# Optimization experiments

Hardware: AMD Instinct MI355X
Metric: run time of the kernel (lower is better)

Reference implementation:

```python
import jax, jax.numpy as jnp
import numpy as np

I = 8      # input size
H = 128    # hidden size
G = 3 * H  # gate rows (reset, update, new)


def setup_inputs() -> dict:
    key = jax.random.key(0)
    ks = jax.random.split(key, 9)
    s = lambda k, shp: (jax.random.normal(k, shp, jnp.float32) * 0.08)
    return {
        "x": jax.random.normal(ks[0], (1, 32768, I), jnp.float32),
        # layer 0 (input 8 -> hidden 128)
        "w_ih0": s(ks[1], (G, I)),
        "w_hh0": s(ks[2], (G, H)),
        "b_ih0": s(ks[3], (G,)),
        "b_hh0": s(ks[4], (G,)),
        # layer 1 (hidden 128 -> hidden 128)
        "w_ih1": s(ks[5], (G, H)),
        "w_hh1": s(ks[6], (G, H)),
        "b_ih1": s(ks[7], (G,)),
        "b_hh1": s(ks[8], (G,)),
    }


def _gru_cell(h, x, w_ih, w_hh, b_ih, b_hh):
    # PyTorch GRU cell math
    gi = x @ w_ih.T + b_ih          # (G,)
    gh = h @ w_hh.T + b_hh          # (G,)
    i_r, i_z, i_n = jnp.split(gi, 3, axis=-1)
    h_r, h_z, h_n = jnp.split(gh, 3, axis=-1)
    r = jax.nn.sigmoid(i_r + h_r)
    z = jax.nn.sigmoid(i_z + h_z)
    n = jnp.tanh(i_n + r * h_n)
    return (1.0 - z) * n + z * h


def reference(x, w_ih0, w_hh0, b_ih0, b_hh0, w_ih1, w_hh1, b_ih1, b_hh1):
    # Torch loop: for k in range(T): feed x[:, k, :] as a length-L sequence
    # (batch=1), carrying hn across chunks. Equivalent flat step order is
    # (k, l) -> index k*L + l, i.e. swapaxes then flatten.
    L, T, _ = x.shape
    seq = jnp.swapaxes(x, 0, 1).reshape(L * T, I)  # (L*T, 8)

    def step(carry, xt):
        h0, h1 = carry
        h0 = _gru_cell(h0, xt, w_ih0, w_hh0, b_ih0, b_hh0)
        h1 = _gru_cell(h1, h0, w_ih1, w_hh1, b_ih1, b_hh1)
        return (h0, h1), h1

    init = (jnp.zeros((H,), x.dtype), jnp.zeros((H,), x.dtype))
    _, outs = jax.lax.scan(step, init, seq)          # (L*T, H)
    # pred from the final chunk: its L top-layer outputs, shape (L, 1, H)
    return outs[-L:].reshape(L, 1, H)
```

## Files before the change

### kernel.cpp

```cpp
#include <hip/hip_runtime.h>


#define T_STEPS 32768
#define HDIM 128
#define CH 1024
#define NC (T_STEPS / CH)
#define GS 8

typedef __attribute__((ext_vector_type(2))) float f32x2;
typedef __attribute__((ext_vector_type(4))) float f32x4;

__device__ __forceinline__ f32x2 lo2(f32x4 v) { return __builtin_shufflevector(v, v, 0, 1); }
__device__ __forceinline__ f32x2 hi2(f32x4 v) { return __builtin_shufflevector(v, v, 2, 3); }
__device__ __forceinline__ void pkfma(f32x2& acc, f32x2 a, f32x2 b) {
  asm("v_pk_fma_f32 %0, %1, %2, %0" : "+v"(acc) : "v"(a), "v"(b));
}
__device__ __forceinline__ float red8(float v) {
  int t = __builtin_amdgcn_mov_dpp(__builtin_bit_cast(int, v), 0xB1, 0xF, 0xF, true);
  v += __builtin_bit_cast(float, t);
  t = __builtin_amdgcn_mov_dpp(__builtin_bit_cast(int, v), 0x4E, 0xF, 0xF, true);
  v += __builtin_bit_cast(float, t);
  t = __builtin_amdgcn_mov_dpp(__builtin_bit_cast(int, v), 0x141, 0xF, 0xF, true);
  v += __builtin_bit_cast(float, t);
  return v;
}

__global__ __launch_bounds__(256)
void gru_prep(const float* __restrict__ w_ih0, const float* __restrict__ w_hh0,
              const float* __restrict__ b_ih0, const float* __restrict__ b_hh0,
              const float* __restrict__ w_ih1, const float* __restrict__ w_hh1,
              const float* __restrict__ b_ih1, const float* __restrict__ b_hh1,
              float* __restrict__ W0s, float* __restrict__ W1s,
              float* __restrict__ Wi0s, float* __restrict__ Wi1s,
              float* __restrict__ bA0, float* __restrict__ bA1,
              float* __restrict__ bhnS0, float* __restrict__ bhnS1) {
  const float SRZ = -1.4426950408889634f;
  const float SN  =  2.8853900817779268f;
  const int i = blockIdx.x * 256 + threadIdx.x;
  if (i < 49152) {
    const float s = ((i >> 7) < 256) ? SRZ : SN;
    W0s[i]  = w_hh0[i] * s;
    W1s[i]  = w_hh1[i] * s;
    Wi1s[i] = w_ih1[i] * s;
  }
  if (i < 3072) Wi0s[i] = w_ih0[i] * (((i >> 3) < 256) ? SRZ : SN);
  if (i < 384) {
    bA0[i] = (i < 256) ? SRZ * (b_ih0[i] + b_hh0[i]) : SN * b_ih0[i];
    bA1[i] = (i < 256) ? SRZ * (b_ih1[i] + b_hh1[i]) : SN * b_ih1[i];
  }
  if (i < 128) {
    bhnS0[i] = SN * b_hh0[256 + i];
    bhnS1[i] = SN * b_hh1[256 + i];
  }
}

#define PKM(D, A, B) "v_pk_mul_f32 v[" D "], v[" A "], v[" B "]\n\t"
#define PKF(D, A, B) "v_pk_fma_f32 v[" D "], v[" A "], v[" B "], v[" D "]\n\t"

#define DOTROW_A(ACC, W0, W1, W2, W3) \
  PKM(ACC, W0, "60:61") PKF(ACC, W1, "62:63") \
  PKF(ACC, W2, "64:65") PKF(ACC, W3, "66:67")
#define DOTROW_B(ACC, W4, W5, W6, W7) \
  PKF(ACC, W4, "68:69") PKF(ACC, W5, "70:71") \
  PKF(ACC, W6, "72:73") PKF(ACC, W7, "74:75")

#define DOTS6_A \
  DOTROW_A("76:77","100:101","102:103","104:105","106:107") \
  DOTROW_A("78:79","116:117","118:119","120:121","122:123") \
  DOTROW_A("80:81","132:133","134:135","136:137","138:139") \
  DOTROW_A("82:83","148:149","150:151","152:153","154:155") \
  DOTROW_A("84:85","164:165","166:167","168:169","170:171") \
  DOTROW_A("86:87","180:181","182:183","184:185","186:187")
#define DOTS6_B \
  DOTROW_B("76:77","108:109","110:111","112:113","114:115") \
  DOTROW_B("78:79","124:125","126:127","128:129","130:131") \
  DOTROW_B("80:81","140:141","142:143","144:145","146:147") \
  DOTROW_B("82:83","156:157","158:159","160:161","162:163") \
  DOTROW_B("84:85","172:173","174:175","176:177","178:179") \
  DOTROW_B("86:87","188:189","190:191","192:193","194:195")

#define RED6 \
  "v_add_f32 v50, v76, v77\n\t" "v_add_f32 v51, v78, v79\n\t" \
  "v_add_f32 v52, v80, v81\n\t" "v_add_f32 v53, v82, v83\n\t" \
  "v_add_f32 v54, v84, v85\n\t" "v_add_f32 v55, v86, v87\n\t" \
  "v_add_f32 v50, v50, v50 quad_perm:[1,0,3,2]\n\t" \
  "v_add_f32 v51, v51, v51 quad_perm:[1,0,3,2]\n\t" \
  "v_add_f32 v52, v52, v52 quad_perm:[1,0,3,2]\n\t" \
  "v_add_f32 v53, v53, v53 quad_perm:[1,0,3,2]\n\t" \
  "v_add_f32 v54, v54, v54 quad_perm:[1,0,3,2]\n\t" \
  "v_add_f32 v55, v55, v55 quad_perm:[1,0,3,2]\n\t" \
  "v_add_f32 v50, v50, v50 quad_perm:[2,3,0,1]\n\t" \
  "v_add_f32 v51, v51, v51 quad_perm:[2,3,0,1]\n\t" \
  "v_add_f32 v52, v52, v52 quad_perm:[2,3,0,1]\n\t" \
  "v_add_f32 v53, v53, v53 quad_perm:[2,3,0,1]\n\t" \
  "v_add_f32 v54, v54, v54 quad_perm:[2,3,0,1]\n\t" \
  "v_add_f32 v55, v55, v55 quad_perm:[2,3,0,1]\n\t" \
  "v_add_f32 v50, v50, v50 row_half_mirror\n\t" \
  "v_add_f32 v51, v51, v51 row_half_mirror\n\t" \
  "v_add_f32 v52, v52, v52 row_half_mirror\n\t" \
  "v_add_f32 v53, v53, v53 row_half_mirror\n\t" \
  "v_add_f32 v54, v54, v54 row_half_mirror\n\t" \
  "v_add_f32 v55, v55, v55 row_half_mirror\n\t"

#define GATES_SPEC(RIN, ZIN, NIN) \
  "v_cndmask_b32 v56, v50, v51, %[mk]\n\t" \
  "v_cndmask_b32 v57, v52, v53, %[mk]\n\t" \
  "v_cndmask_b32 v58, v54, v55, %[mk]\n\t" \
  "v_add_f32 v56, " RIN ", v56\n\t" \
  "v_add_f32 v57, " ZIN ", v57\n\t" \
  "v_add_f32 v58, %[bh], v58\n\t" \
  "v_exp_f32 v56, v56\n\t" \
  "v_exp_f32 v57, v57\n\t" \
  "s_nop 0\n\t" \
  "v_add_f32 v56, 1.0, v56\n\t" \
  "v_add_f32 v57, 1.0, v57\n\t" \
  "v_rcp_f32 v56, v56\n\t" \
  "v_rcp_f32 v57, v57\n\t" \
  "s_nop 0\n\t" \
  "v_fma_f32 v59, v56, v58, " NIN "\n\t" \
  "v_exp_f32 v59, v59\n\t" \
  "s_nop 1\n\t" \
  "v_add_f32 v59, 1.0, v59\n\t" \
  "v_rcp_f32 v59, v59\n\t" \
  "s_nop 1\n\t" \
  "v_fma_f32 v59, -2.0, v59, 1.0\n\t" \
  "v_sub_f32 v49, v48, v59\n\t" \
  "v_fma_f32 v48, v57, v49, v59\n\t"

__device__ __forceinline__ void rec_asm(const float* __restrict__ Ws,
                                        const float* __restrict__ bhnS,
                                        const float* __restrict__ rz,
                                        const float* __restrict__ nb,
                                        float* __restrict__ hstate,
                                        float* __restrict__ h0out,
                                        float* __restrict__ outp, int c) {
  __shared__ __align__(16) float hbuf[2][HDIM];
  __shared__ __align__(16) float hdummy[768];
  const int tid = threadIdx.x, cs = tid & 7, g = tid >> 3;
  const int u0 = 2 * g;
  const int ul = u0 + ((cs & 4) ? 1 : 0);
  float hp = (c > 0) ? hstate[ul] : 0.f;
  const float bh = bhnS[ul];
  unsigned long long mk = __ballot((cs & 4) != 0);
  unsigned vow  = (unsigned)(u0 * 512 + 32 * cs);
  unsigned vow1 = vow + 65536u;
  unsigned vow2 = vow + 131072u;
  unsigned vorz = (unsigned)(2048 + 8 * ul);
  unsigned vonb = (unsigned)(1024 + 4 * ul);
  unsigned voho = (unsigned)(4 * ul);
  unsigned pa = (unsigned)(size_t)&hbuf[0][8 * cs];
  unsigned pw = ((cs & 3) == 0) ? (unsigned)(size_t)&hbuf[0][ul]
                                : (unsigned)(size_t)&hdummy[tid];
  int cnt = CH / 2;

  asm volatile(
    "global_load_dwordx4 v[100:103], %[vow], %[wb]\n\t"
    "global_load_dwordx4 v[104:107], %[vow], %[wb] offset:16\n\t"
    "global_load_dwordx4 v[108:111], %[vow], %[wb] offset:256\n\t"
    "global_load_dwordx4 v[112:115], %[vow], %[wb] offset:272\n\t"
    "global_load_dwordx4 v[116:119], %[vow], %[wb] offset:512\n\t"
    "global_load_dwordx4 v[120:123], %[vow], %[wb] offset:528\n\t"
    "global_load_dwordx4 v[124:127], %[vow], %[wb] offset:768\n\t"
    "global_load_dwordx4 v[128:131], %[vow], %[wb] offset:784\n\t"
    "global_load_dwordx4 v[132:135], %[vow1], %[wb]\n\t"
    "global_load_dwordx4 v[136:139], %[vow1], %[wb] offset:16\n\t"
    "global_load_dwordx4 v[140:143], %[vow1], %[wb] offset:256\n\t"
    "global_load_dwordx4 v[144:147], %[vow1], %[wb] offset:272\n\t"
    "global_load_dwordx4 v[148:151], %[vow1], %[wb] offset:512\n\t"
    "global_load_dwordx4 v[152:155], %[vow1], %[wb] offset:528\n\t"
    "global_load_dwordx4 v[156:159], %[vow1], %[wb] offset:768\n\t"
    "global_load_dwordx4 v[160:163], %[vow1], %[wb] offset:784\n\t"
    "global_load_dwordx4 v[164:167], %[vow2], %[wb]\n\t"
    "global_load_dwordx4 v[168:171], %[vow2], %[wb] offset:16\n\t"
    "global_load_dwordx4 v[172:175], %[vow2], %[wb] offset:256\n\t"
    "global_load_dwordx4 v[176:179], %[vow2], %[wb] offset:272\n\t"
    "global_load_dwordx4 v[180:183], %[vow2], %[wb] offset:512\n\t"
    "global_load_dwordx4 v[184:187], %[vow2], %[wb] offset:528\n\t"
    "global_load_dwordx4 v[188:191], %[vow2], %[wb] offset:768\n\t"
    "global_load_dwordx4 v[192:195], %[vow2], %[wb] offset:784\n\t"
    "global_load_dwordx2 v[88:89], %[vorz], %[rzb] offset:-2048\n\t"
    "global_load_dword v92, %[vonb], %[nbb] offset:-1024\n\t"
    "global_load_dwordx2 v[90:91], %[vorz], %[rzb] offset:-1024\n\t"
    "global_load_dword v93, %[vonb], %[nbb] offset:-512\n\t"
    "v_mov_b32 v48, %[h0]\n\t"
    "ds_write_b32 %[pw], v48\n\t"
    "s_waitcnt vmcnt(0) lgkmcnt(0)\n\t"
    "s_barrier\n\t"
    "Lrec%=:\n\t"
    "ds_read_b128 v[60:63], %[pa]\n\t"
    "ds_read_b128 v[64:67], %[pa] offset:16\n\t"
    "ds_read_b128 v[68:71], %[pa] offset:256\n\t"
    "ds_read_b128 v[72:75], %[pa] offset:272\n\t"
    "s_waitcnt lgkmcnt(2)\n\t"
    DOTS6_A
    "s_waitcnt lgkmcnt(0)\n\t"
    DOTS6_B
    RED6
    "global_load_dwordx2 v[88:89], %[vorz], %[rzb]\n\t"
    "global_load_dword v92, %[vonb], %[nbb]\n\t"
    "s_waitcnt vmcnt(6)\n\t"
    GATES_SPEC("v88", "v89", "v92")
    "ds_write_b32 %[pw], v48 offset:512\n\t"
    "global_store_dword %[voho], v48, %[hob]\n\t"
    "s_waitcnt lgkmcnt(0)\n\t"
    "s_barrier\n\t"
    "ds_read_b128 v[60:63], %[pa] offset:512\n\t"
    "ds_read_b128 v[64:67], %[pa] offset:528\n\t"
    "ds_read_b128 v[68:71], %[pa] offset:768\n\t"
    "ds_read_b128 v[72:75], %[pa] offset:784\n\t"
    "s_waitcnt lgkmcnt(2)\n\t"
    DOTS6_A
    "s_waitcnt lgkmcnt(0)\n\t"
    DOTS6_B
    RED6
    "global_load_dwordx2 v[90:91], %[vorz], %[rzb] offset:1024\n\t"
    "global_load_dword v93, %[vonb], %[nbb] offset:512\n\t"
    "s_waitcnt vmcnt(6)\n\t"
    GATES_SPEC("v90", "v91", "v93")
    "ds_write_b32 %[pw], v48\n\t"
    "global_store_dword %[voho], v48, %[hob] offset:512\n\t"
    "v_add_u32 %[vorz], 2048, %[vorz]\n\t"
    "v_add_u32 %[vonb], 1024, %[vonb]\n\t"
    "v_add_u32 %[voho], 1024, %[voho]\n\t"
    "s_waitcnt lgkmcnt(0)\n\t"
    "s_barrier\n\t"
    "s_sub_u32 %[cnt], %[cnt], 1\n\t"
    "s_cmp_lg_u32 %[cnt], 0\n\t"
    "s_cbranch_scc1 Lrec%=\n\t"
    "v_mov_b32 %[h0], v48\n\t"
    : [vorz]"+v"(vorz), [vonb]"+v"(vonb), [voho]"+v"(voho), [cnt]"+s"(cnt),
      [h0]"+v"(hp)
    : [wb]"s"(Ws), [rzb]"s"(rz), [nbb]"s"(nb), [hob]"s"(h0out),
      [vow]"v"(vow), [vow1]"v"(vow1), [vow2]"v"(vow2),
      [pa]"v"(pa), [pw]"v"(pw), [bh]"v"(bh), [mk]"s"(mk)
    : "memory", "scc",
      "v48","v49","v50","v51","v52","v53","v54","v55","v56","v57","v58","v59",
      "v60","v61","v62","v63","v64","v65","v66","v67","v68","v69","v70","v71",
      "v72","v73","v74","v75","v76","v77","v78","v79","v80","v81","v82","v83",
      "v84","v85","v86","v87","v88","v89","v90","v91","v92","v93","v94","v95",
      "v96","v97","v98","v99","v100","v101","v102","v103","v104","v105","v106",
      "v107","v108","v109","v110","v111","v112","v113","v114","v115","v116",
      "v117","v118","v119","v120","v121","v122","v123","v124","v125","v126",
      "v127","v128","v129","v130","v131","v132","v133","v134","v135","v136",
      "v137","v138","v139","v140","v141","v142","v143","v144","v145","v146",
      "v147","v148","v149","v150","v151","v152","v153","v154","v155","v156",
      "v157","v158","v159","v160","v161","v162","v163","v164","v165","v166",
      "v167","v168","v169","v170","v171","v172","v173","v174","v175","v176",
      "v177","v178","v179","v180","v181","v182","v183","v184","v185","v186",
      "v187","v188","v189","v190","v191","v192","v193","v194","v195");

  if ((cs & 3) == 0) {
    hstate[ul] = hp;
    if (outp) outp[ul] = hp;
  }
}

__device__ __forceinline__ void role_giA(int rb, int c, const float* __restrict__ x,
                                         const float* __restrict__ Wi0s,
                                         const float* __restrict__ bA0,
                                         float* __restrict__ rz, float* __restrict__ nb) {
  const int tid = threadIdx.x;
  const int u = tid & 127, sb = tid >> 7;
  const int row = rb * 128 + u;
  const f32x4 wa = *(const f32x4*)(Wi0s + (size_t)row * 8);
  const f32x4 wb = *(const f32x4*)(Wi0s + (size_t)row * 8 + 4);
  const float bias = bA0[row];
  const int m = u >> 1, sub = u & 1;
  for (int i = 0; i < CH / 4; ++i) {
    const int tl = sb * (CH / 4) + i;
    const float* xp = x + ((size_t)c * CH + tl) * 8;
    const f32x4 xa = *(const f32x4*)xp;
    const f32x4 xb2 = *(const f32x4*)(xp + 4);
    float acc = bias;
    acc = fmaf(wa.x, xa.x, acc); acc = fmaf(wa.y, xa.y, acc);
    acc = fmaf(wa.z, xa.z, acc); acc = fmaf(wa.w, xa.w, acc);
    acc = fmaf(wb.x, xb2.x, acc); acc = fmaf(wb.y, xb2.y, acc);
    acc = fmaf(wb.z, xb2.z, acc); acc = fmaf(wb.w, xb2.w, acc);
    if (rb < 2) rz[(size_t)tl * 256 + 4 * m + 2 * sub + rb] = acc;
    else        nb[(size_t)tl * 128 + u] = acc;
  }
}

__device__ __forceinline__ void role_giB(int rb, const float* __restrict__ h0src,
                                         const float* __restrict__ Wi1s,
                                         const float* __restrict__ bA1,
                                         float* __restrict__ rz, float* __restrict__ nb) {
  __shared__ __align__(16) float hsg[2][GS * HDIM];
  const int tid = threadIdx.x, cs = tid & 7, m = tid >> 3;
  const int R0 = rb * 128 + 2 * m, R1 = R0 + 1;
  f32x4 V0[4], V1[4];
  {
    const float* p0 = Wi1s + (size_t)R0 * 128 + 8 * cs;
    const float* p1 = Wi1s + (size_t)R1 * 128 + 8 * cs;
    V0[0] = *(const f32x4*)p0;        V0[1] = *(const f32x4*)(p0 + 4);
    V0[2] = *(const f32x4*)(p0 + 64); V0[3] = *(const f32x4*)(p0 + 68);
    V1[0] = *(const f32x4*)p1;        V1[1] = *(const f32x4*)(p1 + 4);
    V1[2] = *(const f32x4*)(p1 + 64); V1[3] = *(const f32x4*)(p1 + 68);
  }
  const float b0 = bA1[R0], b1 = bA1[R1];

  if (tid < 256) ((f32x4*)hsg[0])[tid] = ((const f32x4*)h0src)[tid];
  __syncthreads();
  int cur = 0;
  for (int gb = 0; gb < CH / GS; ++gb) {
    f32x4 pf;
    const bool hv = (gb + 1 < CH / GS) && (tid < 256);
    if (hv) pf = ((const f32x4*)(h0src + (size_t)(gb + 1) * (GS * HDIM)))[tid];
    #pragma unroll
    for (int s = 0; s < GS; ++s) {
      const float* hb = hsg[cur] + s * HDIM;
      const f32x4 hA = *(const f32x4*)(hb + 8 * cs);
      const f32x4 hB = *(const f32x4*)(hb + 8 * cs + 4);
      const f32x4 hC = *(const f32x4*)(hb + 64 + 8 * cs);
      const f32x4 hD = *(const f32x4*)(hb + 64 + 8 * cs + 4);
      f32x2 d0 = {0.f, 0.f}, d1 = d0;
      pkfma(d0, lo2(V0[0]), lo2(hA)); pkfma(d0, hi2(V0[0]), hi2(hA));
      pkfma(d0, lo2(V0[1]), lo2(hB)); pkfma(d0, hi2(V0[1]), hi2(hB));
      pkfma(d0, lo2(V0[2]), lo2(hC)); pkfma(d0, hi2(V0[2]), hi2(hC));
      pkfma(d0, lo2(V0[3]), lo2(hD)); pkfma(d0, hi2(V0[3]), hi2(hD));
      pkfma(d1, lo2(V1[0]), lo2(hA)); pkfma(d1, hi2(V1[0]), hi2(hA));
      pkfma(d1, lo2(V1[1]), lo2(hB)); pkfma(d1, hi2(V1[1]), hi2(hB));
      pkfma(d1, lo2(V1[2]), lo2(hC)); pkfma(d1, hi2(V1[2]), hi2(hC));
      pkfma(d1, lo2(V1[3]), lo2(hD)); pkfma(d1, hi2(V1[3]), hi2(hD));
      const float a0 = red8(d0.x + d0.y) + b0;
      const float a1 = red8(d1.x + d1.y) + b1;
      if (cs == 0) {
        const int tl = gb * GS + s;
        if (rb < 2) {
          rz[(size_t)tl * 256 + 4 * m + rb] = a0;
          rz[(size_t)tl * 256 + 4 * m + 2 + rb] = a1;
        } else {
          f32x2 nv = {a0, a1};
          *(f32x2*)(nb + (size_t)tl * 128 + 2 * m) = nv;
        }
      }
    }
    if (hv) ((f32x4*)hsg[cur ^ 1])[tid] = pf;
    __syncthreads();
    cur ^= 1;
  }
}

__global__ __launch_bounds__(512)
void gru_pipe(const float* __restrict__ x, float* __restrict__ out,
              const float* __restrict__ W0s, const float* __restrict__ W1s,
              const float* __restrict__ Wi0s, const float* __restrict__ Wi1s,
              const float* __restrict__ bA0, const float* __restrict__ bA1,
              const float* __restrict__ bhnS0, const float* __restrict__ bhnS1,
              float* __restrict__ hstate0, float* __restrict__ hstate1,
              float* __restrict__ h0ring, float* __restrict__ gi0rz,
              float* __restrict__ gi0n, float* __restrict__ gi1rz,
              float* __restrict__ gi1n, float* __restrict__ h1dump, int k) {
  const int bid = blockIdx.x;
  if (bid == 0) {
    const int c = k - 1;
    if (c >= 0 && c < NC)
      rec_asm(W0s, bhnS0,
              gi0rz + (size_t)(c & 1) * CH * 256, gi0n + (size_t)(c & 1) * CH * 128,
              hstate0, h0ring + (size_t)(c & 1) * CH * HDIM, nullptr, c);
  } else if (bid == 1) {
    const int c = k - 3;
    if (c >= 0 && c < NC)
      rec_asm(W1s, bhnS1,
              gi1rz + (size_t)(c & 1) * CH * 256, gi1n + (size_t)(c & 1) * CH * 128,
              hstate1, h1dump, (c == NC - 1) ? out : nullptr, c);
  } else {
    const int rb = bid - 2;
    if (k < NC)
      role_giA(rb, k, x, Wi0s, bA0,
               gi0rz + (size_t)(k & 1) * CH * 256, gi0n + (size_t)(k & 1) * CH * 128);
    const int cb = k - 2;
    if (cb >= 0 && cb < NC)
      role_giB(rb, h0ring + (size_t)(cb & 1) * CH * HDIM, Wi1s, bA1,
               gi1rz + (size_t)(cb & 1) * CH * 256, gi1n + (size_t)(cb & 1) * CH * 128);
  }
}

extern "C" void kernel_launch(void* const* d_in, const int* in_sizes, int n_in,
                              void* d_out, int out_size, void* d_ws, size_t ws_size,
                              hipStream_t stream) {
  (void)in_sizes; (void)n_in; (void)out_size; (void)ws_size;
  const float* x     = (const float*)d_in[0];
  const float* w_ih0 = (const float*)d_in[1];
  const float* w_hh0 = (const float*)d_in[2];
  const float* b_ih0 = (const float*)d_in[3];
  const float* b_hh0 = (const float*)d_in[4];
  const float* w_ih1 = (const float*)d_in[5];
  const float* w_hh1 = (const float*)d_in[6];
  const float* b_ih1 = (const float*)d_in[7];
  const float* b_hh1 = (const float*)d_in[8];
  float* out = (float*)d_out;

  float* p = (float*)d_ws;
  float* W0s    = p; p += 49152;
  float* W1s    = p; p += 49152;
  float* Wi1s   = p; p += 49152;
  float* Wi0s   = p; p += 3072;
  float* bA0    = p; p += 384;
  float* bA1    = p; p += 384;
  float* bhnS0  = p; p += 128;
  float* bhnS1  = p; p += 128;
  float* hstate0 = p; p += 128;
  float* hstate1 = p; p += 128;
  float* h0ring  = p; p += (size_t)2 * CH * 128;
  float* gi0rz   = p; p += (size_t)2 * CH * 256;
  float* gi0n    = p; p += (size_t)2 * CH * 128;
  float* gi1rz   = p; p += (size_t)2 * CH * 256;
  float* gi1n    = p; p += (size_t)2 * CH * 128;
  float* h1dump  = p; p += (size_t)CH * 128;

  hipLaunchKernelGGL(gru_prep, dim3(192), dim3(256), 0, stream,
                     w_ih0, w_hh0, b_ih0, b_hh0, w_ih1, w_hh1, b_ih1, b_hh1,
                     W0s, W1s, Wi0s, Wi1s, bA0, bA1, bhnS0, bhnS1);
  for (int k = 0; k <= NC + 2; ++k) {
    hipLaunchKernelGGL(gru_pipe, dim3(5), dim3(512), 0, stream,
                       x, out, W0s, W1s, Wi0s, Wi1s, bA0, bA1, bhnS0, bhnS1,
                       hstate0, hstate1, h0ring, gi0rz, gi0n, gi1rz, gi1n,
                       h1dump, k);
  }
}
```

Measured before the change: 16.31 ms.

## Halve recurrent threads to 256 with 4-lane dot splits and padded LDS

```diff
diff --git a/kernel.cpp b/kernel.cpp
--- a/kernel.cpp
+++ b/kernel.cpp
@@ -57,75 +57,71 @@
 #define PKM(D, A, B) "v_pk_mul_f32 v[" D "], v[" A "], v[" B "]\n\t"
 #define PKF(D, A, B) "v_pk_fma_f32 v[" D "], v[" A "], v[" B "], v[" D "]\n\t"
 
-#define DOTROW_A(ACC, W0, W1, W2, W3) \
-  PKM(ACC, W0, "60:61") PKF(ACC, W1, "62:63") \
-  PKF(ACC, W2, "64:65") PKF(ACC, W3, "66:67")
-#define DOTROW_B(ACC, W4, W5, W6, W7) \
-  PKF(ACC, W4, "68:69") PKF(ACC, W5, "70:71") \
-  PKF(ACC, W6, "72:73") PKF(ACC, W7, "74:75")
-
-#define DOTS6_A \
-  DOTROW_A("76:77","100:101","102:103","104:105","106:107") \
-  DOTROW_A("78:79","116:117","118:119","120:121","122:123") \
-  DOTROW_A("80:81","132:133","134:135","136:137","138:139") \
-  DOTROW_A("82:83","148:149","150:151","152:153","154:155") \
-  DOTROW_A("84:85","164:165","166:167","168:169","170:171") \
-  DOTROW_A("86:87","180:181","182:183","184:185","186:187")
-#define DOTS6_B \
-  DOTROW_B("76:77","108:109","110:111","112:113","114:115") \
-  DOTROW_B("78:79","124:125","126:127","128:129","130:131") \
-  DOTROW_B("80:81","140:141","142:143","144:145","146:147") \
-  DOTROW_B("82:83","156:157","158:159","160:161","162:163") \
-  DOTROW_B("84:85","172:173","174:175","176:177","178:179") \
-  DOTROW_B("86:87","188:189","190:191","192:193","194:195")
-
-#define RED6 \
-  "v_add_f32 v50, v76, v77\n\t" "v_add_f32 v51, v78, v79\n\t" \
-  "v_add_f32 v52, v80, v81\n\t" "v_add_f32 v53, v82, v83\n\t" \
-  "v_add_f32 v54, v84, v85\n\t" "v_add_f32 v55, v86, v87\n\t" \
-  "v_add_f32 v50, v50, v50 quad_perm:[1,0,3,2]\n\t" \
-  "v_add_f32 v51, v51, v51 quad_perm:[1,0,3,2]\n\t" \
-  "v_add_f32 v52, v52, v52 quad_perm:[1,0,3,2]\n\t" \
-  "v_add_f32 v53, v53, v53 quad_perm:[1,0,3,2]\n\t" \
-  "v_add_f32 v54, v54, v54 quad_perm:[1,0,3,2]\n\t" \
-  "v_add_f32 v55, v55, v55 quad_perm:[1,0,3,2]\n\t" \
-  "v_add_f32 v50, v50, v50 quad_perm:[2,3,0,1]\n\t" \
-  "v_add_f32 v51, v51, v51 quad_perm:[2,3,0,1]\n\t" \
-  "v_add_f32 v52, v52, v52 quad_perm:[2,3,0,1]\n\t" \
-  "v_add_f32 v53, v53, v53 quad_perm:[2,3,0,1]\n\t" \
-  "v_add_f32 v54, v54, v54 quad_perm:[2,3,0,1]\n\t" \
-  "v_add_f32 v55, v55, v55 quad_perm:[2,3,0,1]\n\t" \
-  "v_add_f32 v50, v50, v50 row_half_mirror\n\t" \
-  "v_add_f32 v51, v51, v51 row_half_mirror\n\t" \
-  "v_add_f32 v52, v52, v52 row_half_mirror\n\t" \
-  "v_add_f32 v53, v53, v53 row_half_mirror\n\t" \
-  "v_add_f32 v54, v54, v54 row_half_mirror\n\t" \
-  "v_add_f32 v55, v55, v55 row_half_mirror\n\t"
-
-#define GATES_SPEC(RIN, ZIN, NIN) \
-  "v_cndmask_b32 v56, v50, v51, %[mk]\n\t" \
-  "v_cndmask_b32 v57, v52, v53, %[mk]\n\t" \
-  "v_cndmask_b32 v58, v54, v55, %[mk]\n\t" \
-  "v_add_f32 v56, " RIN ", v56\n\t" \
-  "v_add_f32 v57, " ZIN ", v57\n\t" \
-  "v_add_f32 v58, %[bh], v58\n\t" \
-  "v_exp_f32 v56, v56\n\t" \
-  "v_exp_f32 v57, v57\n\t" \
+#define ROW8A(OP0, ACC, W0, W1, W2, W3, W4, W5, W6, W7) \
+  OP0(ACC, W0, "32:33") PKF(ACC, W1, "34:35") PKF(ACC, W2, "36:37") \
+  PKF(ACC, W3, "38:39") PKF(ACC, W4, "40:41") PKF(ACC, W5, "42:43") \
+  PKF(ACC, W6, "44:45") PKF(ACC, W7, "46:47")
+#define ROW8B(ACC, W0, W1, W2, W3, W4, W5, W6, W7) \
+  PKF(ACC, W0, "48:49") PKF(ACC, W1, "50:51") PKF(ACC, W2, "52:53") \
+  PKF(ACC, W3, "54:55") PKF(ACC, W4, "56:57") PKF(ACC, W5, "58:59") \
+  PKF(ACC, W6, "60:61") PKF(ACC, W7, "62:63")
+
+#define DOTS_A \
+  ROW8A(PKM, "20:21", "64:65","66:67","68:69","70:71","72:73","74:75","76:77","78:79") \
+  ROW8A(PKM, "22:23", "96:97","98:99","100:101","102:103","104:105","106:107","108:109","110:111") \
+  ROW8A(PKM, "24:25", "128:129","130:131","132:133","134:135","136:137","138:139","140:141","142:143") \
+  ROW8A(PKM, "26:27", "160:161","162:163","164:165","166:167","168:169","170:171","172:173","174:175") \
+  ROW8A(PKM, "28:29", "192:193","194:195","196:197","198:199","200:201","202:203","204:205","206:207") \
+  ROW8A(PKM, "30:31", "224:225","226:227","228:229","230:231","232:233","234:235","236:237","238:239")
+#define DOTS_B \
+  ROW8B("20:21", "80:81","82:83","84:85","86:87","88:89","90:91","92:93","94:95") \
+  ROW8B("22:23", "112:113","114:115","116:117","118:119","120:121","122:123","124:125","126:127") \
+  ROW8B("24:25", "144:145","146:147","148:149","150:151","152:153","154:155","156:157","158:159") \
+  ROW8B("26:27", "176:177","178:179","180:181","182:183","184:185","186:187","188:189","190:191") \
+  ROW8B("28:29", "208:209","210:211","212:213","214:215","216:217","218:219","220:221","222:223") \
+  ROW8B("30:31", "240:241","242:243","244:245","246:247","248:249","250:251","252:253","254:255")
+
+#define RED2 \
+  "v_add_f32 v32, v20, v21\n\t" "v_add_f32 v33, v22, v23\n\t" \
+  "v_add_f32 v34, v24, v25\n\t" "v_add_f32 v35, v26, v27\n\t" \
+  "v_add_f32 v36, v28, v29\n\t" "v_add_f32 v37, v30, v31\n\t" \
+  "v_add_f32 v32, v32, v32 quad_perm:[1,0,3,2]\n\t" \
+  "v_add_f32 v33, v33, v33 quad_perm:[1,0,3,2]\n\t" \
+  "v_add_f32 v34, v34, v34 quad_perm:[1,0,3,2]\n\t" \
+  "v_add_f32 v35, v35, v35 quad_perm:[1,0,3,2]\n\t" \
+  "v_add_f32 v36, v36, v36 quad_perm:[1,0,3,2]\n\t" \
+  "v_add_f32 v37, v37, v37 quad_perm:[1,0,3,2]\n\t" \
+  "v_add_f32 v32, v32, v32 quad_perm:[2,3,0,1]\n\t" \
+  "v_add_f32 v33, v33, v33 quad_perm:[2,3,0,1]\n\t" \
+  "v_add_f32 v34, v34, v34 quad_perm:[2,3,0,1]\n\t" \
+  "v_add_f32 v35, v35, v35 quad_perm:[2,3,0,1]\n\t" \
+  "v_add_f32 v36, v36, v36 quad_perm:[2,3,0,1]\n\t" \
+  "v_add_f32 v37, v37, v37 quad_perm:[2,3,0,1]\n\t" \
+  "v_cndmask_b32 v38, v32, v33, %[mk]\n\t" \
+  "v_cndmask_b32 v39, v34, v35, %[mk]\n\t" \
+  "v_cndmask_b32 v40, v36, v37, %[mk]\n\t"
+
+#define GATES1(RIN, ZIN, NIN) \
+  "v_add_f32 v41, " RIN ", v38\n\t" \
+  "v_add_f32 v42, " ZIN ", v39\n\t" \
+  "v_add_f32 v43, %[bh], v40\n\t" \
+  "v_exp_f32 v41, v41\n\t" \
+  "v_exp_f32 v42, v42\n\t" \
   "s_nop 0\n\t" \
-  "v_add_f32 v56, 1.0, v56\n\t" \
-  "v_add_f32 v57, 1.0, v57\n\t" \
-  "v_rcp_f32 v56, v56\n\t" \
-  "v_rcp_f32 v57, v57\n\t" \
+  "v_add_f32 v41, 1.0, v41\n\t" \
+  "v_add_f32 v42, 1.0, v42\n\t" \
+  "v_rcp_f32 v41, v41\n\t" \
+  "v_rcp_f32 v42, v42\n\t" \
   "s_nop 0\n\t" \
-  "v_fma_f32 v59, v56, v58, " NIN "\n\t" \
-  "v_exp_f32 v59, v59\n\t" \
+  "v_fma_f32 v44, v41, v43, " NIN "\n\t" \
+  "v_exp_f32 v44, v44\n\t" \
   "s_nop 1\n\t" \
-  "v_add_f32 v59, 1.0, v59\n\t" \
-  "v_rcp_f32 v59, v59\n\t" \
+  "v_add_f32 v44, 1.0, v44\n\t" \
+  "v_rcp_f32 v44, v44\n\t" \
   "s_nop 1\n\t" \
-  "v_fma_f32 v59, -2.0, v59, 1.0\n\t" \
-  "v_sub_f32 v49, v48, v59\n\t" \
-  "v_fma_f32 v48, v57, v49, v59\n\t"
+  "v_fma_f32 v44, -2.0, v44, 1.0\n\t" \
+  "v_sub_f32 v43, %[h0], v44\n\t" \
+  "v_fma_f32 %[h0], v42, v43, v44\n\t"
 
 __device__ __forceinline__ void rec_asm(const float* __restrict__ Ws,
                                         const float* __restrict__ bhnS,
@@ -134,91 +130,123 @@
                                         float* __restrict__ hstate,
                                         float* __restrict__ h0out,
                                         float* __restrict__ outp, int c) {
-  __shared__ __align__(16) float hbuf[2][HDIM];
-  __shared__ __align__(16) float hdummy[768];
-  const int tid = threadIdx.x, cs = tid & 7, g = tid >> 3;
+  __shared__ __align__(16) float hbuf[2][144];
+  __shared__ __align__(16) float hdummy[256];
+  const int tid = threadIdx.x, cs = tid & 3, g = tid >> 2;
   const int u0 = 2 * g;
-  const int ul = u0 + ((cs & 4) ? 1 : 0);
+  const int ul = u0 + ((cs & 2) >> 1);
   float hp = (c > 0) ? hstate[ul] : 0.f;
   const float bh = bhnS[ul];
-  unsigned long long mk = __ballot((cs & 4) != 0);
-  unsigned vow  = (unsigned)(u0 * 512 + 32 * cs);
-  unsigned vow1 = vow + 65536u;
-  unsigned vow2 = vow + 131072u;
+  unsigned long long mk = __ballot((cs & 2) != 0);
+  const unsigned wrd = (unsigned)(ul + 4 * (ul >> 5));
+  unsigned vow  = (unsigned)(u0 * 512 + 128 * cs);
   unsigned vorz = (unsigned)(2048 + 8 * ul);
   unsigned vonb = (unsigned)(1024 + 4 * ul);
   unsigned voho = (unsigned)(4 * ul);
-  unsigned pa = (unsigned)(size_t)&hbuf[0][8 * cs];
-  unsigned pw = ((cs & 3) == 0) ? (unsigned)(size_t)&hbuf[0][ul]
+  unsigned pa = (unsigned)(size_t)&hbuf[0][36 * cs];
+  unsigned pw = ((cs & 1) == 0) ? (unsigned)(size_t)&hbuf[0][wrd]
                                 : (unsigned)(size_t)&hdummy[tid];
   int cnt = CH / 2;
 
   asm volatile(
-    "global_load_dwordx4 v[100:103], %[vow], %[wb]\n\t"
-    "global_load_dwordx4 v[104:107], %[vow], %[wb] offset:16\n\t"
-    "global_load_dwordx4 v[108:111], %[vow], %[wb] offset:256\n\t"
-    "global_load_dwordx4 v[112:115], %[vow], %[wb] offset:272\n\t"
-    "global_load_dwordx4 v[116:119], %[vow], %[wb] offset:512\n\t"
-    "global_load_dwordx4 v[120:123], %[vow], %[wb] offset:528\n\t"
-    "global_load_dwordx4 v[124:127], %[vow], %[wb] offset:768\n\t"
-    "global_load_dwordx4 v[128:131], %[vow], %[wb] offset:784\n\t"
-    "global_load_dwordx4 v[132:135], %[vow1], %[wb]\n\t"
-    "global_load_dwordx4 v[136:139], %[vow1], %[wb] offset:16\n\t"
-    "global_load_dwordx4 v[140:143], %[vow1], %[wb] offset:256\n\t"
-    "global_load_dwordx4 v[144:147], %[vow1], %[wb] offset:272\n\t"
-    "global_load_dwordx4 v[148:151], %[vow1], %[wb] offset:512\n\t"
-    "global_load_dwordx4 v[152:155], %[vow1], %[wb] offset:528\n\t"
-    "global_load_dwordx4 v[156:159], %[vow1], %[wb] offset:768\n\t"
-    "global_load_dwordx4 v[160:163], %[vow1], %[wb] offset:784\n\t"
-    "global_load_dwordx4 v[164:167], %[vow2], %[wb]\n\t"
-    "global_load_dwordx4 v[168:171], %[vow2], %[wb] offset:16\n\t"
-    "global_load_dwordx4 v[172:175], %[vow2], %[wb] offset:256\n\t"
-    "global_load_dwordx4 v[176:179], %[vow2], %[wb] offset:272\n\t"
-    "global_load_dwordx4 v[180:183], %[vow2], %[wb] offset:512\n\t"
-    "global_load_dwordx4 v[184:187], %[vow2], %[wb] offset:528\n\t"
-    "global_load_dwordx4 v[188:191], %[vow2], %[wb] offset:768\n\t"
-    "global_load_dwordx4 v[192:195], %[vow2], %[wb] offset:784\n\t"
-    "global_load_dwordx2 v[88:89], %[vorz], %[rzb] offset:-2048\n\t"
-    "global_load_dword v92, %[vonb], %[nbb] offset:-1024\n\t"
-    "global_load_dwordx2 v[90:91], %[vorz], %[rzb] offset:-1024\n\t"
-    "global_load_dword v93, %[vonb], %[nbb] offset:-512\n\t"
-    "v_mov_b32 v48, %[h0]\n\t"
-    "ds_write_b32 %[pw], v48\n\t"
+    "v_add_u32 v45, 0x10000, %[vow]\n\t"
+    "v_add_u32 v46, 0x20000, %[vow]\n\t"
+    "global_load_dwordx4 v[64:67], %[vow], %[wb]\n\t"
+    "global_load_dwordx4 v[68:71], %[vow], %[wb] offset:16\n\t"
+    "global_load_dwordx4 v[72:75], %[vow], %[wb] offset:32\n\t"
+    "global_load_dwordx4 v[76:79], %[vow], %[wb] offset:48\n\t"
+    "global_load_dwordx4 v[80:83], %[vow], %[wb] offset:64\n\t"
+    "global_load_dwordx4 v[84:87], %[vow], %[wb] offset:80\n\t"
+    "global_load_dwordx4 v[88:91], %[vow], %[wb] offset:96\n\t"
+    "global_load_dwordx4 v[92:95], %[vow], %[wb] offset:112\n\t"
+    "global_load_dwordx4 v[96:99], %[vow], %[wb] offset:512\n\t"
+    "global_load_dwordx4 v[100:103], %[vow], %[wb] offset:528\n\t"
+    "global_load_dwordx4 v[104:107], %[vow], %[wb] offset:544\n\t"
+    "global_load_dwordx4 v[108:111], %[vow], %[wb] offset:560\n\t"
+    "global_load_dwordx4 v[112:115], %[vow], %[wb] offset:576\n\t"
+    "global_load_dwordx4 v[116:119], %[vow], %[wb] offset:592\n\t"
+    "global_load_dwordx4 v[120:123], %[vow], %[wb] offset:608\n\t"
+    "global_load_dwordx4 v[124:127], %[vow], %[wb] offset:624\n\t"
+    "global_load_dwordx4 v[128:131], v45, %[wb]\n\t"
+    "global_load_dwordx4 v[132:135], v45, %[wb] offset:16\n\t"
+    "global_load_dwordx4 v[136:139], v45, %[wb] offset:32\n\t"
+    "global_load_dwordx4 v[140:143], v45, %[wb] offset:48\n\t"
+    "global_load_dwordx4 v[144:147], v45, %[wb] offset:64\n\t"
+    "global_load_dwordx4 v[148:151], v45, %[wb] offset:80\n\t"
+    "global_load_dwordx4 v[152:155], v45, %[wb] offset:96\n\t"
+    "global_load_dwordx4 v[156:159], v45, %[wb] offset:112\n\t"
+    "global_load_dwordx4 v[160:163], v45, %[wb] offset:512\n\t"
+    "global_load_dwordx4 v[164:167], v45, %[wb] offset:528\n\t"
+    "global_load_dwordx4 v[168:171], v45, %[wb] offset:544\n\t"
+    "global_load_dwordx4 v[172:175], v45, %[wb] offset:560\n\t"
+    "global_load_dwordx4 v[176:179], v45, %[wb] offset:576\n\t"
+    "global_load_dwordx4 v[180:183], v45, %[wb] offset:592\n\t"
+    "global_load_dwordx4 v[184:187], v45, %[wb] offset:608\n\t"
+    "global_load_dwordx4 v[188:191], v45, %[wb] offset:624\n\t"
+    "global_load_dwordx4 v[192:195], v46, %[wb]\n\t"
+    "global_load_dwordx4 v[196:199], v46, %[wb] offset:16\n\t"
+    "global_load_dwordx4 v[200:203], v46, %[wb] offset:32\n\t"
+    "global_load_dwordx4 v[204:207], v46, %[wb] offset:48\n\t"
+    "global_load_dwordx4 v[208:211], v46, %[wb] offset:64\n\t"
+    "global_load_dwordx4 v[212:215], v46, %[wb] offset:80\n\t"
+    "global_load_dwordx4 v[216:219], v46, %[wb] offset:96\n\t"
+    "global_load_dwordx4 v[220:223], v46, %[wb] offset:112\n\t"
+    "global_load_dwordx4 v[224:227], v46, %[wb] offset:512\n\t"
+    "global_load_dwordx4 v[228:231], v46, %[wb] offset:528\n\t"
+    "global_load_dwordx4 v[232:235], v46, %[wb] offset:544\n\t"
+    "global_load_dwordx4 v[236:239], v46, %[wb] offset:560\n\t"
+    "global_load_dwordx4 v[240:243], v46, %[wb] offset:576\n\t"
+    "global_load_dwordx4 v[244:247], v46, %[wb] offset:592\n\t"
+    "global_load_dwordx4 v[248:251], v46, %[wb] offset:608\n\t"
+    "global_load_dwordx4 v[252:255], v46, %[wb] offset:624\n\t"
+    "global_load_dwordx2 v[12:13], %[vorz], %[rzb] offset:-2048\n\t"
+    "global_load_dword v14, %[vonb], %[nbb] offset:-1024\n\t"
+    "global_load_dwordx2 v[16:17], %[vorz], %[rzb] offset:-1024\n\t"
+    "global_load_dword v18, %[vonb], %[nbb] offset:-512\n\t"
+    "ds_write_b32 %[pw], %[h0]\n\t"
     "s_waitcnt vmcnt(0) lgkmcnt(0)\n\t"
     "s_barrier\n\t"
     "Lrec%=:\n\t"
-    "ds_read_b128 v[60:63], %[pa]\n\t"
-    "ds_read_b128 v[64:67], %[pa] offset:16\n\t"
-    "ds_read_b128 v[68:71], %[pa] offset:256\n\t"
-    "ds_read_b128 v[72:75], %[pa] offset:272\n\t"
-    "s_waitcnt lgkmcnt(2)\n\t"
-    DOTS6_A
+    "ds_read_b128 v[32:35], %[pa]\n\t"
+    "ds_read_b128 v[36:39], %[pa] offset:16\n\t"
+    "ds_read_b128 v[40:43], %[pa] offset:32\n\t"
+    "ds_read_b128 v[44:47], %[pa] offset:48\n\t"
+    "ds_read_b128 v[48:51], %[pa] offset:64\n\t"
+    "ds_read_b128 v[52:55], %[pa] offset:80\n\t"
+    "ds_read_b128 v[56:59], %[pa] offset:96\n\t"
+    "ds_read_b128 v[60:63], %[pa] offset:112\n\t"
+    "s_waitcnt lgkmcnt(4)\n\t"
+    DOTS_A
     "s_waitcnt lgkmcnt(0)\n\t"
-    DOTS6_B
-    RED6
-    "global_load_dwordx2 v[88:89], %[vorz], %[rzb]\n\t"
-    "global_load_dword v92, %[vonb], %[nbb]\n\t"
-    "s_waitcnt vmcnt(6)\n\t"
-    GATES_SPEC("v88", "v89", "v92")
-    "ds_write_b32 %[pw], v48 offset:512\n\t"
-    "global_store_dword %[voho], v48, %[hob]\n\t"
+    DOTS_B
+    RED2
+    "s_waitcnt vmcnt(2)\n\t"
+    GATES1("v12", "v13", "v14")
+    "global_load_dwordx2 v[12:13], %[vorz], %[rzb]\n\t"
+    "global_load_dword v14, %[vonb], %[nbb]\n\t"
+    "ds_write_b32 %[pw], %[h0] offset:576\n\t"
+    "global_store_dword %[voho], %[h0], %[hob]\n\t"
     "s_waitcnt lgkmcnt(0)\n\t"
     "s_barrier\n\t"
-    "ds_read_b128 v[60:63], %[pa] offset:512\n\t"
-    "ds_read_b128 v[64:67], %[pa] offset:528\n\t"
-    "ds_read_b128 v[68:71], %[pa] offset:768\n\t"
-    "ds_read_b128 v[72:75], %[pa] offset:784\n\t"
-    "s_waitcnt lgkmcnt(2)\n\t"
-    DOTS6_A
+    "ds_read_b128 v[32:35], %[pa] offset:576\n\t"
+    "ds_read_b128 v[36:39], %[pa] offset:592\n\t"
+    "ds_read_b128 v[40:43], %[pa] offset:608\n\t"
+    "ds_read_b128 v[44:47], %[pa] offset:624\n\t"
+    "ds_read_b128 v[48:51], %[pa] offset:640\n\t"
+    "ds_read_b128 v[52:55], %[pa] offset:656\n\t"
+    "ds_read_b128 v[56:59], %[pa] offset:672\n\t"
+    "ds_read_b128 v[60:63], %[pa] offset:688\n\t"
+    "s_waitcnt lgkmcnt(4)\n\t"
+    DOTS_A
     "s_waitcnt lgkmcnt(0)\n\t"
-    DOTS6_B
-    RED6
-    "global_load_dwordx2 v[90:91], %[vorz], %[rzb] offset:1024\n\t"
-    "global_load_dword v93, %[vonb], %[nbb] offset:512\n\t"
-    "s_waitcnt vmcnt(6)\n\t"
-    GATES_SPEC("v90", "v91", "v93")
-    "ds_write_b32 %[pw], v48\n\t"
-    "global_store_dword %[voho], v48, %[hob] offset:512\n\t"
+    DOTS_B
+    RED2
+    "s_waitcnt vmcnt(2)\n\t"
+    GATES1("v16", "v17", "v18")
+    "global_load_dwordx2 v[16:17], %[vorz], %[rzb] offset:1024\n\t"
+    "global_load_dword v18, %[vonb], %[nbb] offset:512\n\t"
+    "ds_write_b32 %[pw], %[h0]\n\t"
+    "global_store_dword %[voho], %[h0], %[hob] offset:512\n\t"
     "v_add_u32 %[vorz], 2048, %[vorz]\n\t"
     "v_add_u32 %[vonb], 1024, %[vonb]\n\t"
     "v_add_u32 %[voho], 1024, %[voho]\n\t"
@@ -227,32 +255,46 @@
     "s_sub_u32 %[cnt], %[cnt], 1\n\t"
     "s_cmp_lg_u32 %[cnt], 0\n\t"
     "s_cbranch_scc1 Lrec%=\n\t"
-    "v_mov_b32 %[h0], v48\n\t"
     : [vorz]"+v"(vorz), [vonb]"+v"(vonb), [voho]"+v"(voho), [cnt]"+s"(cnt),
       [h0]"+v"(hp)
     : [wb]"s"(Ws), [rzb]"s"(rz), [nbb]"s"(nb), [hob]"s"(h0out),
-      [vow]"v"(vow), [vow1]"v"(vow1), [vow2]"v"(vow2),
-      [pa]"v"(pa), [pw]"v"(pw), [bh]"v"(bh), [mk]"s"(mk)
+      [vow]"v"(vow), [pa]"v"(pa), [pw]"v"(pw), [bh]"v"(bh), [mk]"s"(mk)
     : "memory", "scc",
-      "v48","v49","v50","v51","v52","v53","v54","v55","v56","v57","v58","v59",
-      "v60","v61","v62","v63","v64","v65","v66","v67","v68","v69","v70","v71",
-      "v72","v73","v74","v75","v76","v77","v78","v79","v80","v81","v82","v83",
-      "v84","v85","v86","v87","v88","v89","v90","v91","v92","v93","v94","v95",
-      "v96","v97","v98","v99","v100","v101","v102","v103","v104","v105","v106",
-      "v107","v108","v109","v110","v111","v112","v113","v114","v115","v116",
-      "v117","v118","v119","v120","v121","v122","v123","v124","v125","v126",
-      "v127","v128","v129","v130","v131","v132","v133","v134","v135","v136",
-      "v137","v138","v139","v140","v141","v142","v143","v144","v145","v146",
-      "v147","v148","v149","v150","v151","v152","v153","v154","v155","v156",
-      "v157","v158","v159","v160","v161","v162","v163","v164","v165","v166",
-      "v167","v168","v169","v170","v171","v172","v173","v174","v175","v176",
-      "v177","v178","v179","v180","v181","v182","v183","v184","v185","v186",
-      "v187","v188","v189","v190","v191","v192","v193","v194","v195");
-
-  if ((cs & 3) == 0) {
+      "v12","v13","v14","v15","v16","v17","v18","v19",
+      "v20","v21","v22","v23","v24","v25","v26","v27","v28","v29","v30","v31",
+      "v32","v33","v34","v35","v36","v37","v38","v39","v40","v41","v42","v43",
+      "v44","v45","v46","v47","v48","v49","v50","v51","v52","v53","v54","v55",
+      "v56","v57","v58","v59","v60","v61","v62","v63","v64","v65","v66","v67",
+      "v68","v69","v70","v71","v72","v73","v74","v75","v76","v77","v78","v79",
+      "v80","v81","v82","v83","v84","v85","v86","v87","v88","v89","v90","v91",
+      "v92","v93","v94","v95","v96","v97","v98","v99","v100","v101","v102",
+      "v103","v104","v105","v106","v107","v108","v109","v110","v111","v112",
+      "v113","v114","v115","v116","v117","v118","v119","v120","v121","v122",
+      "v123","v124","v125","v126","v127","v128","v129","v130","v131","v132",
+      "v133","v134","v135","v136","v137","v138","v139","v140","v141","v142",
+      "v143","v144","v145","v146","v147","v148","v149","v150","v151","v152",
+      "v153","v154","v155","v156","v157","v158","v159","v160","v161","v162",
+      "v163","v164","v165","v166","v167","v168","v169","v170","v171","v172",
+      "v173","v174","v175","v176","v177","v178","v179","v180","v181","v182",
+      "v183","v184","v185","v186","v187","v188","v189","v190","v191","v192",
+      "v193","v194","v195","v196","v197","v198","v199","v200","v201","v202",
+      "v203","v204","v205","v206","v207","v208","v209","v210","v211","v212",
+      "v213","v214","v215","v216","v217","v218","v219","v220","v221","v222",
+      "v223","v224","v225","v226","v227","v228","v229","v230","v231","v232",
+      "v233","v234","v235","v236","v237","v238","v239","v240","v241","v242",
+      "v243","v244","v245","v246","v247","v248","v249","v250","v251","v252",
+      "v253","v254","v255");
+
+  if ((cs & 1) == 0) {
     hstate[ul] = hp;
     if (outp) outp[ul] = hp;
   }
+}
+
+__device__ __forceinline__ void idle_barriers() {
+  #pragma unroll 1
+  for (int i = 0; i <= CH; ++i)
+    asm volatile("s_barrier" ::: "memory");
 }
 
 __device__ __forceinline__ void role_giA(int rb, int c, const float* __restrict__ x,
@@ -354,16 +396,24 @@
   const int bid = blockIdx.x;
   if (bid == 0) {
     const int c = k - 1;
-    if (c >= 0 && c < NC)
-      rec_asm(W0s, bhnS0,
-              gi0rz + (size_t)(c & 1) * CH * 256, gi0n + (size_t)(c & 1) * CH * 128,
-              hstate0, h0ring + (size_t)(c & 1) * CH * HDIM, nullptr, c);
+    if (c >= 0 && c < NC) {
+      if (threadIdx.x < 256)
+        rec_asm(W0s, bhnS0,
+                gi0rz + (size_t)(c & 1) * CH * 256, gi0n + (size_t)(c & 1) * CH * 128,
+                hstate0, h0ring + (size_t)(c & 1) * CH * HDIM, nullptr, c);
+      else
+        idle_barriers();
+    }
   } else if (bid == 1) {
     const int c = k - 3;
-    if (c >= 0 && c < NC)
-      rec_asm(W1s, bhnS1,
-              gi1rz + (size_t)(c & 1) * CH * 256, gi1n + (size_t)(c & 1) * CH * 128,
-              hstate1, h1dump, (c == NC - 1) ? out : nullptr, c);
+    if (c >= 0 && c < NC) {
+      if (threadIdx.x < 256)
+        rec_asm(W1s, bhnS1,
+                gi1rz + (size_t)(c & 1) * CH * 256, gi1n + (size_t)(c & 1) * CH * 128,
+                hstate1, h1dump, (c == NC - 1) ? out : nullptr, c);
+      else
+        idle_barriers();
+    }
   } else {
     const int rb = bid - 2;
     if (k < NC)
```

Result: faster. 14.45 ms (-11.4%).
